# Kernel tuning notes

Hardware: AMD Instinct MI355X
Metric: run time of the kernel (lower is better)

The kernel has to match this reference:

```python
import jax, jax.numpy as jnp
import numpy as np

N_NODES = 100000


def _gcn_norm(edge_index, num_nodes):
    # add self loops, then symmetric normalization D^-1/2 (A+I) D^-1/2
    loops = jnp.arange(num_nodes, dtype=edge_index.dtype)
    src = jnp.concatenate([edge_index[0], loops])
    dst = jnp.concatenate([edge_index[1], loops])
    ones = jnp.ones(src.shape[0], dtype=jnp.float32)
    deg = jax.ops.segment_sum(ones, dst, num_segments=num_nodes)
    dinv = jnp.where(deg > 0, jax.lax.rsqrt(deg), 0.0)
    norm = dinv[src] * dinv[dst]  # [E+N]
    return src, dst, norm


def setup_inputs() -> dict:
    key = jax.random.key(0)
    k1, k2, k3, k4 = jax.random.split(key, 4)
    x = jax.random.normal(k1, (N_NODES, 512), dtype=jnp.float32)
    edge_index = jax.random.randint(k2, (2, 3200000), 0, N_NODES, dtype=jnp.int64)
    # SGConv linear: Linear(num_features=512, num_classes=40)
    W = jax.random.normal(k3, (40, 512), dtype=jnp.float32) / np.sqrt(512.0)
    b = jax.random.normal(k4, (40,), dtype=jnp.float32) * 0.01
    return {"x": x, "edge_index": edge_index, "W": W, "b": b}


def reference(x, edge_index, W, b):
    K = 2  # args.num_layers
    src, dst, norm = _gcn_norm(edge_index, N_NODES)
    h = x
    for _ in range(K):
        # SpMM: out[dst] += norm * h[src]
        h = jax.ops.segment_sum(norm[:, None] * h[src], dst, num_segments=N_NODES)
    logits = h @ W.T + b  # [N, num_classes]
    return jax.nn.log_softmax(logits, axis=1)
```

## Files before the change

kernel.cpp:

```cpp
#include <hip/hip_runtime.h>
#include <hip/hip_bf16.h>
#include <math.h>


#define NFEAT 512
#define NCLS  40
#define NBUCK_MAX 512
#define CAP   9728

typedef __attribute__((ext_vector_type(8))) short bf16x8;
typedef __attribute__((ext_vector_type(4))) float f32x4;

__device__ inline short f2bf(float f) {
    union { float f; unsigned u; } v; v.f = f;
    unsigned r = (v.u + 0x7FFFu + ((v.u >> 16) & 1u)) >> 16;
    return (short)r;
}
__device__ inline unsigned pack2bf(float a, float b) {
    return (unsigned)(unsigned short)f2bf(a) | ((unsigned)(unsigned short)f2bf(b) << 16);
}
__device__ inline float bflo(unsigned v) {
    union { unsigned u; float f; } r; r.u = v << 16; return r.f;
}
__device__ inline float bfhi(unsigned v) {
    union { unsigned u; float f; } r; r.u = v & 0xFFFF0000u; return r.f;
}


__global__ __launch_bounds__(256) void scat7_kernel(const int* __restrict__ src,
                                                    const int* __restrict__ dst,
                                                    int* __restrict__ bcursor,
                                                    unsigned* __restrict__ bco, int E) {
    __shared__ int h[NBUCK_MAX], h2[NBUCK_MAX], base[NBUCK_MAX];
    int t = threadIdx.x;
    h[t] = 0; h[t + 256] = 0; h2[t] = 0; h2[t + 256] = 0;
    __syncthreads();
    int cb = blockIdx.x * 2048;
    int d[8], s[8];
    bool m[8];
    #pragma unroll
    for (int u = 0; u < 8; ++u) {
        int e = cb + u * 256 + t;
        m[u] = e < E;
        d[u] = m[u] ? __builtin_nontemporal_load(dst + e) : 0;
        s[u] = m[u] ? __builtin_nontemporal_load(src + e) : 0;
        if (m[u]) atomicAdd(&h[d[u] >> 8], 1);
    }
    __syncthreads();
    #pragma unroll
    for (int b = 0; b < 2; ++b) {
        int bb = t + b * 256;
        if (h[bb]) base[bb] = bb * CAP + atomicAdd(&bcursor[bb], h[bb]);
    }
    __syncthreads();
    #pragma unroll
    for (int u = 0; u < 8; ++u) {
        if (m[u]) {
            int b = d[u] >> 8;
            int lp = atomicAdd(&h2[b], 1);
            bco[base[b] + lp] = ((unsigned)s[u] << 8) | (unsigned)(d[u] & 255);
        }
    }
}


__global__ __launch_bounds__(256) void sortb3_kernel(const unsigned* __restrict__ bco,
                                                     const int* __restrict__ bcursor,
                                                     int4* __restrict__ rowinfo,
                                                     float* __restrict__ dinv,
                                                     int* __restrict__ csr_src, int N) {
    __shared__ int deg[256], ex[256], sc[256];
    int b = blockIdx.x, t = threadIdx.x;
    int lo = b * 256;
    int nn = N - lo; if (nn > 256) nn = 256;
    int ebeg = b * CAP;
    int ecnt = bcursor[b];

    deg[t] = 0;
    __syncthreads();
    for (int i = t; i < ecnt; i += 256)
        atomicAdd(&deg[bco[ebeg + i] & 255u], 1);
    __syncthreads();
    int v = deg[t];
    sc[t] = v;
    __syncthreads();
    for (int off = 1; off < 256; off <<= 1) {
        int u = (t >= off) ? sc[t - off] : 0;
        __syncthreads();
        sc[t] += u;
        __syncthreads();
    }
    int ext = sc[t] - v;
    ex[t] = ext;
    if (t < nn) {
        float di = rsqrtf((float)(v + 1));
        int4 ri;
        ri.x = ebeg + ext;
        ri.y = v;
        ri.z = __float_as_int(di);
        ri.w = 0;
        rowinfo[lo + t] = ri;
        dinv[lo + t]    = di;
    }
    __syncthreads();
    for (int i = t; i < ecnt; i += 256) {
        unsigned e = bco[ebeg + i];
        int p = atomicAdd(&ex[e & 255u], 1);
        csr_src[ebeg + p] = (int)(e >> 8);
    }
}


__global__ void wfrag_kernel(const float* __restrict__ W, short* __restrict__ wfrag,
                             int* __restrict__ bcursor) {
    int i = blockIdx.x * blockDim.x + threadIdx.x;
    if (i < NBUCK_MAX) bcursor[i] = 0;
    if (i >= 16 * 3 * 64) return;
    int kc = i / 192, rem = i % 192, tile = rem / 64, lane = rem % 64;
    int c = tile * 16 + (lane & 15);
    int kbase = kc * 32 + ((lane >> 4) << 3);
    bf16x8 out;
    #pragma unroll
    for (int j = 0; j < 8; ++j) {
        float v = (c < NCLS) ? W[(size_t)c * NFEAT + kbase + j] : 0.f;
        out[j] = f2bf(v);
    }
    *(bf16x8*)(wfrag + (size_t)i * 8) = out;
}


__global__ __launch_bounds__(512) void gemm7_kernel(const float* __restrict__ x,
                                                    const short* __restrict__ wfrag,
                                                    const float* __restrict__ dinv,
                                                    unsigned short* __restrict__ zp, int n) {
    __shared__ short xl[2][128 * 40];
    int t = threadIdx.x;
    int w = t >> 6, l = t & 63;
    int lrow = l & 15, lk = l >> 4;
    int rowBase = blockIdx.x * 128;
    int srow = t >> 2, skq = t & 3;
    f32x4 acc0 = {0.f, 0.f, 0.f, 0.f}, acc1 = acc0, acc2 = acc0;
    const float* xrow = x + (size_t)(rowBase + srow) * NFEAT + skq * 8;
    bool srOK = (rowBase + srow) < n;
    int aoff = (w * 16 + lrow) * 40 + lk * 8;
    int doff = srow * 40 + skq * 8;

    {
        float4 v0 = make_float4(0.f, 0.f, 0.f, 0.f), v1 = v0;
        if (srOK) { const float4* xp = (const float4*)xrow; v0 = xp[0]; v1 = xp[1]; }
        bf16x8 bv;
        bv[0] = f2bf(v0.x); bv[1] = f2bf(v0.y); bv[2] = f2bf(v0.z); bv[3] = f2bf(v0.w);
        bv[4] = f2bf(v1.x); bv[5] = f2bf(v1.y); bv[6] = f2bf(v1.z); bv[7] = f2bf(v1.w);
        *(bf16x8*)&xl[0][doff] = bv;
    }
    __syncthreads();

    for (int kc = 0; kc < 16; ++kc) {
        int cur = kc & 1;
        float4 v0 = make_float4(0.f, 0.f, 0.f, 0.f), v1 = v0;
        if (kc < 15 && srOK) {
            const float4* xp = (const float4*)(xrow + (kc + 1) * 32);
            v0 = xp[0]; v1 = xp[1];
        }
        bf16x8 af = *(const bf16x8*)&xl[cur][aoff];
        const bf16x8* wf = (const bf16x8*)(wfrag + (size_t)kc * 3 * 64 * 8);
        bf16x8 b0 = wf[l];
        bf16x8 b1 = wf[64 + l];
        bf16x8 b2 = wf[128 + l];
        acc0 = __builtin_amdgcn_mfma_f32_16x16x32_bf16(af, b0, acc0, 0, 0, 0);
        acc1 = __builtin_amdgcn_mfma_f32_16x16x32_bf16(af, b1, acc1, 0, 0, 0);
        acc2 = __builtin_amdgcn_mfma_f32_16x16x32_bf16(af, b2, acc2, 0, 0, 0);
        if (kc < 15) {
            bf16x8 bv;
            bv[0] = f2bf(v0.x); bv[1] = f2bf(v0.y); bv[2] = f2bf(v0.z); bv[3] = f2bf(v0.w);
            bv[4] = f2bf(v1.x); bv[5] = f2bf(v1.y); bv[6] = f2bf(v1.z); bv[7] = f2bf(v1.w);
            *(bf16x8*)&xl[cur ^ 1][doff] = bv;
            __syncthreads();
        }
    }
    int r0 = rowBase + w * 16 + lk * 4;
    #pragma unroll
    for (int reg = 0; reg < 4; ++reg) {
        int row = r0 + reg;
        if (row < n) {
            float sc = dinv[row];
            unsigned short* zr = zp + (size_t)row * 64;
            zr[lrow]      = (unsigned short)f2bf(acc0[reg] * sc);
            zr[16 + lrow] = (unsigned short)f2bf(acc1[reg] * sc);
            zr[32 + lrow] = (lrow < 8) ? (unsigned short)f2bf(acc2[reg] * sc) : 0;
            zr[48 + lrow] = 0;
        }
    }
}


template <bool FINAL>
__global__ __launch_bounds__(256) void spmm12_kernel(const unsigned short* __restrict__ in,
                                                     const int4* __restrict__ rowinfo,
                                                     const int* __restrict__ csr,
                                                     const float* __restrict__ bias,
                                                     unsigned short* __restrict__ outP,
                                                     float* __restrict__ outF, int n) {
    int wv = (int)((blockIdx.x * (size_t)blockDim.x + threadIdx.x) >> 6);
    wv = __builtin_amdgcn_readfirstlane(wv);
    if (wv >= n) return;
    int lane = threadIdx.x & 63;
    int g  = lane >> 3;
    int oc = lane & 7;

    const char* rowb = (const char*)in + oc * 16;

    int4 ri = rowinfo[wv];
    int beg = ri.x, tot = ri.y;
    float dd = __int_as_float(ri.z);

    float a0 = 0.f, a1 = 0.f, a2 = 0.f, a3 = 0.f,
          a4 = 0.f, a5 = 0.f, a6 = 0.f, a7 = 0.f;

#define ACC_ADD(V)                                                     \
    { a0 += bflo((V).x); a1 += bfhi((V).x); a2 += bflo((V).y);         \
      a3 += bfhi((V).y); a4 += bflo((V).z); a5 += bfhi((V).z);         \
      a6 += bflo((V).w); a7 += bfhi((V).w); }

    if (g == 0) {
        uint4 v = *(const uint4*)(rowb + (size_t)wv * 128);
        ACC_ADD(v);
    }

    int j = 0;
    for (; j + 32 <= tot; j += 32) {
        int s0 = csr[beg + j + g];
        int s1 = csr[beg + j + 8 + g];
        int s2 = csr[beg + j + 16 + g];
        int s3 = csr[beg + j + 24 + g];
        uint4 v0 = *(const uint4*)(rowb + (size_t)s0 * 128);
        uint4 v1 = *(const uint4*)(rowb + (size_t)s1 * 128);
        uint4 v2 = *(const uint4*)(rowb + (size_t)s2 * 128);
        uint4 v3 = *(const uint4*)(rowb + (size_t)s3 * 128);
        ACC_ADD(v0); ACC_ADD(v1); ACC_ADD(v2); ACC_ADD(v3);
    }
    for (; j < tot; j += 8) {
        if (g < tot - j) {
            int s = csr[beg + j + g];
            uint4 v = *(const uint4*)(rowb + (size_t)s * 128);
            ACC_ADD(v);
        }
    }
#undef ACC_ADD

    #pragma unroll
    for (int off = 8; off <= 32; off <<= 1) {
        a0 += __shfl_xor(a0, off, 64); a1 += __shfl_xor(a1, off, 64);
        a2 += __shfl_xor(a2, off, 64); a3 += __shfl_xor(a3, off, 64);
        a4 += __shfl_xor(a4, off, 64); a5 += __shfl_xor(a5, off, 64);
        a6 += __shfl_xor(a6, off, 64); a7 += __shfl_xor(a7, off, 64);
    }

    if (!FINAL) {
        if (g == 0) {
            float s2 = dd * dd;
            uint4 o;
            o.x = pack2bf(a0 * s2, a1 * s2);
            o.y = pack2bf(a2 * s2, a3 * s2);
            o.z = pack2bf(a4 * s2, a5 * s2);
            o.w = pack2bf(a6 * s2, a7 * s2);
            *(uint4*)((char*)outP + (size_t)wv * 128 + oc * 16) = o;
        }
    } else {
        float b0 = 0.f, b1 = 0.f, b2 = 0.f, b3 = 0.f,
              b4 = 0.f, b5 = 0.f, b6 = 0.f, b7 = 0.f;
        if (oc < 5) {
            float4 q0 = ((const float4*)bias)[oc * 2];
            float4 q1 = ((const float4*)bias)[oc * 2 + 1];
            b0 = q0.x; b1 = q0.y; b2 = q0.z; b3 = q0.w;
            b4 = q1.x; b5 = q1.y; b6 = q1.z; b7 = q1.w;
        }
        bool valid = oc < 5;
        float v0 = valid ? a0 * dd + b0 : -INFINITY;
        float v1 = valid ? a1 * dd + b1 : -INFINITY;
        float v2 = valid ? a2 * dd + b2 : -INFINITY;
        float v3 = valid ? a3 * dd + b3 : -INFINITY;
        float v4 = valid ? a4 * dd + b4 : -INFINITY;
        float v5 = valid ? a5 * dd + b5 : -INFINITY;
        float v6 = valid ? a6 * dd + b6 : -INFINITY;
        float v7 = valid ? a7 * dd + b7 : -INFINITY;
        float m = fmaxf(fmaxf(fmaxf(v0, v1), fmaxf(v2, v3)),
                        fmaxf(fmaxf(v4, v5), fmaxf(v6, v7)));
        #pragma unroll
        for (int off = 1; off <= 4; off <<= 1) m = fmaxf(m, __shfl_xor(m, off, 64));
        float es = 0.f;
        if (valid)
            es = expf(v0 - m) + expf(v1 - m) + expf(v2 - m) + expf(v3 - m)
               + expf(v4 - m) + expf(v5 - m) + expf(v6 - m) + expf(v7 - m);
        #pragma unroll
        for (int off = 1; off <= 4; off <<= 1) es += __shfl_xor(es, off, 64);
        float lse = logf(es) + m;
        if (g == 0 && valid) {
            float* op = outF + (size_t)wv * NCLS + oc * 8;
            float4 o0 = make_float4(v0 - lse, v1 - lse, v2 - lse, v3 - lse);
            float4 o1 = make_float4(v4 - lse, v5 - lse, v6 - lse, v7 - lse);
            *(float4*)op = o0;
            *(float4*)(op + 4) = o1;
        }
    }
}


extern "C" void kernel_launch(void* const* d_in, const int* in_sizes, int n_in,
                              void* d_out, int out_size, void* d_ws, size_t ws_size,
                              hipStream_t stream) {
    const float* x  = (const float*)d_in[0];
    const int*   ei = (const int*)d_in[1];
    const float* W  = (const float*)d_in[2];
    const float* b  = (const float*)d_in[3];

    const int N = in_sizes[0] / NFEAT;
    const int E = in_sizes[1] / 2;
    const int* src = ei;
    const int* dst = ei + E;
    const int nbuck = (N + 255) >> 8;

    char* p = (char*)d_ws;
    auto alloc = [&](size_t bytes) -> void* {
        void* r = (void*)p;
        p += (bytes + 255) & ~(size_t)255;
        return r;
    };
    int*      bcursor = (int*)     alloc((size_t)NBUCK_MAX * 4);
    int4*     rowinfo = (int4*)    alloc((size_t)N * 16);
    float*    dinv    = (float*)   alloc((size_t)N * 4);
    unsigned* bco     = (unsigned*)alloc((size_t)nbuck * CAP * 4 + 64);
    int*      csr_src = (int*)     alloc((size_t)nbuck * CAP * 4 + 64);
    short*    wfrag   = (short*)   alloc((size_t)16 * 3 * 64 * 8 * 2);
    unsigned short* zp  = (unsigned short*)alloc((size_t)N * 64 * 2);
    unsigned short* h1p = (unsigned short*)alloc((size_t)N * 64 * 2);

    wfrag_kernel<<<12, 256, 0, stream>>>(W, wfrag, bcursor);

    int cb = (E + 2047) / 2048;
    scat7_kernel<<<cb, 256, 0, stream>>>(src, dst, bcursor, bco, E);
    sortb3_kernel<<<nbuck, 256, 0, stream>>>(bco, bcursor, rowinfo, dinv, csr_src, N);

    gemm7_kernel<<<(N + 127) / 128, 512, 0, stream>>>(x, wfrag, dinv, zp, N);

    int wb = (int)(((size_t)N * 64 + 255) / 256);
    spmm12_kernel<false><<<wb, 256, 0, stream>>>(zp, rowinfo, csr_src, b, h1p, nullptr, N);
    spmm12_kernel<true ><<<wb, 256, 0, stream>>>(h1p, rowinfo, csr_src, b, nullptr,
                                                 (float*)d_out, N);
}
```

Measured before the change: 259.1 us.

## Fuse edge scatter with x·W GEMM in one launch and defer dinv scaling

The edge bucketing scatter and the dense x·W^T GEMM now run as separate block ranges of a single kernel, so the memory-bound scatter and the GEMM can overlap instead of running back to back. GEMM blocks are shrunk to 64 rows with 256 threads so both roles share one launch shape. Since the GEMM no longer waits for degrees, the dinv row scaling moves into the sort kernel, which rescales zp in place after building the CSR. This adds an extra read-modify-write pass over zp in the sort kernel, and the smaller GEMM tiles may reuse the W fragments less.

```diff
diff --git a/kernel.cpp b/kernel.cpp
--- a/kernel.cpp
+++ b/kernel.cpp
@@ -24,90 +24,6 @@
 }
 __device__ inline float bfhi(unsigned v) {
     union { unsigned u; float f; } r; r.u = v & 0xFFFF0000u; return r.f;
-}
-
-
-__global__ __launch_bounds__(256) void scat7_kernel(const int* __restrict__ src,
-                                                    const int* __restrict__ dst,
-                                                    int* __restrict__ bcursor,
-                                                    unsigned* __restrict__ bco, int E) {
-    __shared__ int h[NBUCK_MAX], h2[NBUCK_MAX], base[NBUCK_MAX];
-    int t = threadIdx.x;
-    h[t] = 0; h[t + 256] = 0; h2[t] = 0; h2[t + 256] = 0;
-    __syncthreads();
-    int cb = blockIdx.x * 2048;
-    int d[8], s[8];
-    bool m[8];
-    #pragma unroll
-    for (int u = 0; u < 8; ++u) {
-        int e = cb + u * 256 + t;
-        m[u] = e < E;
-        d[u] = m[u] ? __builtin_nontemporal_load(dst + e) : 0;
-        s[u] = m[u] ? __builtin_nontemporal_load(src + e) : 0;
-        if (m[u]) atomicAdd(&h[d[u] >> 8], 1);
-    }
-    __syncthreads();
-    #pragma unroll
-    for (int b = 0; b < 2; ++b) {
-        int bb = t + b * 256;
-        if (h[bb]) base[bb] = bb * CAP + atomicAdd(&bcursor[bb], h[bb]);
-    }
-    __syncthreads();
-    #pragma unroll
-    for (int u = 0; u < 8; ++u) {
-        if (m[u]) {
-            int b = d[u] >> 8;
-            int lp = atomicAdd(&h2[b], 1);
-            bco[base[b] + lp] = ((unsigned)s[u] << 8) | (unsigned)(d[u] & 255);
-        }
-    }
-}
-
-
-__global__ __launch_bounds__(256) void sortb3_kernel(const unsigned* __restrict__ bco,
-                                                     const int* __restrict__ bcursor,
-                                                     int4* __restrict__ rowinfo,
-                                                     float* __restrict__ dinv,
-                                                     int* __restrict__ csr_src, int N) {
-    __shared__ int deg[256], ex[256], sc[256];
-    int b = blockIdx.x, t = threadIdx.x;
-    int lo = b * 256;
-    int nn = N - lo; if (nn > 256) nn = 256;
-    int ebeg = b * CAP;
-    int ecnt = bcursor[b];
-
-    deg[t] = 0;
-    __syncthreads();
-    for (int i = t; i < ecnt; i += 256)
-        atomicAdd(&deg[bco[ebeg + i] & 255u], 1);
-    __syncthreads();
-    int v = deg[t];
-    sc[t] = v;
-    __syncthreads();
-    for (int off = 1; off < 256; off <<= 1) {
-        int u = (t >= off) ? sc[t - off] : 0;
-        __syncthreads();
-        sc[t] += u;
-        __syncthreads();
-    }
-    int ext = sc[t] - v;
-    ex[t] = ext;
-    if (t < nn) {
-        float di = rsqrtf((float)(v + 1));
-        int4 ri;
-        ri.x = ebeg + ext;
-        ri.y = v;
-        ri.z = __float_as_int(di);
-        ri.w = 0;
-        rowinfo[lo + t] = ri;
-        dinv[lo + t]    = di;
-    }
-    __syncthreads();
-    for (int i = t; i < ecnt; i += 256) {
-        unsigned e = bco[ebeg + i];
-        int p = atomicAdd(&ex[e & 255u], 1);
-        csr_src[ebeg + p] = (int)(e >> 8);
-    }
 }
 
 
@@ -129,15 +45,57 @@
 }
 
 
-__global__ __launch_bounds__(512) void gemm7_kernel(const float* __restrict__ x,
-                                                    const short* __restrict__ wfrag,
-                                                    const float* __restrict__ dinv,
-                                                    unsigned short* __restrict__ zp, int n) {
-    __shared__ short xl[2][128 * 40];
+__global__ __launch_bounds__(256) void fused1_kernel(const int* __restrict__ src,
+                                                     const int* __restrict__ dst,
+                                                     int* __restrict__ bcursor,
+                                                     unsigned* __restrict__ bco, int E,
+                                                     int CB,
+                                                     const float* __restrict__ x,
+                                                     const short* __restrict__ wfrag,
+                                                     unsigned short* __restrict__ zp,
+                                                     int n) {
+    __shared__ __align__(16) char smem[2 * 64 * 40 * 2];
     int t = threadIdx.x;
+
+    if (blockIdx.x < (unsigned)CB) {
+        int* h    = (int*)smem;
+        int* h2   = h + NBUCK_MAX;
+        int* base = h2 + NBUCK_MAX;
+        h[t] = 0; h[t + 256] = 0; h2[t] = 0; h2[t + 256] = 0;
+        __syncthreads();
+        int cb = blockIdx.x * 2048;
+        int d[8], s[8];
+        bool m[8];
+        #pragma unroll
+        for (int u = 0; u < 8; ++u) {
+            int e = cb + u * 256 + t;
+            m[u] = e < E;
+            d[u] = m[u] ? __builtin_nontemporal_load(dst + e) : 0;
+            s[u] = m[u] ? __builtin_nontemporal_load(src + e) : 0;
+            if (m[u]) atomicAdd(&h[d[u] >> 8], 1);
+        }
+        __syncthreads();
+        #pragma unroll
+        for (int b = 0; b < 2; ++b) {
+            int bb = t + b * 256;
+            if (h[bb]) base[bb] = bb * CAP + atomicAdd(&bcursor[bb], h[bb]);
+        }
+        __syncthreads();
+        #pragma unroll
+        for (int u = 0; u < 8; ++u) {
+            if (m[u]) {
+                int b = d[u] >> 8;
+                int lp = atomicAdd(&h2[b], 1);
+                bco[base[b] + lp] = ((unsigned)s[u] << 8) | (unsigned)(d[u] & 255);
+            }
+        }
+        return;
+    }
+
+    short (*xl)[64 * 40] = (short (*)[64 * 40])smem;
     int w = t >> 6, l = t & 63;
     int lrow = l & 15, lk = l >> 4;
-    int rowBase = blockIdx.x * 128;
+    int rowBase = (blockIdx.x - CB) * 64;
     int srow = t >> 2, skq = t & 3;
     f32x4 acc0 = {0.f, 0.f, 0.f, 0.f}, acc1 = acc0, acc2 = acc0;
     const float* xrow = x + (size_t)(rowBase + srow) * NFEAT + skq * 8;
@@ -183,13 +141,66 @@
     for (int reg = 0; reg < 4; ++reg) {
         int row = r0 + reg;
         if (row < n) {
-            float sc = dinv[row];
             unsigned short* zr = zp + (size_t)row * 64;
-            zr[lrow]      = (unsigned short)f2bf(acc0[reg] * sc);
-            zr[16 + lrow] = (unsigned short)f2bf(acc1[reg] * sc);
-            zr[32 + lrow] = (lrow < 8) ? (unsigned short)f2bf(acc2[reg] * sc) : 0;
+            zr[lrow]      = (unsigned short)f2bf(acc0[reg]);
+            zr[16 + lrow] = (unsigned short)f2bf(acc1[reg]);
+            zr[32 + lrow] = (lrow < 8) ? (unsigned short)f2bf(acc2[reg]) : 0;
             zr[48 + lrow] = 0;
         }
+    }
+}
+
+
+__global__ __launch_bounds__(256) void sortb4_kernel(const unsigned* __restrict__ bco,
+                                                     const int* __restrict__ bcursor,
+                                                     int4* __restrict__ rowinfo,
+                                                     int* __restrict__ csr_src,
+                                                     unsigned short* __restrict__ zp,
+                                                     int N) {
+    __shared__ int deg[256], ex[256], sc[256];
+    int b = blockIdx.x, t = threadIdx.x;
+    int lo = b * 256;
+    int nn = N - lo; if (nn > 256) nn = 256;
+    int ebeg = b * CAP;
+    int ecnt = bcursor[b];
+
+    deg[t] = 0;
+    __syncthreads();
+    for (int i = t; i < ecnt; i += 256)
+        atomicAdd(&deg[bco[ebeg + i] & 255u], 1);
+    __syncthreads();
+    int v = deg[t];
+    sc[t] = v;
+    __syncthreads();
+    for (int off = 1; off < 256; off <<= 1) {
+        int u = (t >= off) ? sc[t - off] : 0;
+        __syncthreads();
+        sc[t] += u;
+        __syncthreads();
+    }
+    int ext = sc[t] - v;
+    ex[t] = ext;
+    if (t < nn) {
+        float di = rsqrtf((float)(v + 1));
+        int4 ri;
+        ri.x = ebeg + ext;
+        ri.y = v;
+        ri.z = __float_as_int(di);
+        ri.w = 0;
+        rowinfo[lo + t] = ri;
+    }
+    __syncthreads();
+    for (int i = t; i < ecnt; i += 256) {
+        unsigned e = bco[ebeg + i];
+        int p = atomicAdd(&ex[e & 255u], 1);
+        csr_src[ebeg + p] = (int)(e >> 8);
+    }
+    for (int idx = t; idx < nn * 32; idx += 256) {
+        int row = idx >> 5, c = idx & 31;
+        float di = rsqrtf((float)(deg[row] + 1));
+        unsigned* zr = (unsigned*)(zp + (size_t)(lo + row) * 64);
+        unsigned vv = zr[c];
+        zr[c] = pack2bf(bflo(vv) * di, bfhi(vv) * di);
     }
 }
 
@@ -328,7 +339,6 @@
     };
     int*      bcursor = (int*)     alloc((size_t)NBUCK_MAX * 4);
     int4*     rowinfo = (int4*)    alloc((size_t)N * 16);
-    float*    dinv    = (float*)   alloc((size_t)N * 4);
     unsigned* bco     = (unsigned*)alloc((size_t)nbuck * CAP * 4 + 64);
     int*      csr_src = (int*)     alloc((size_t)nbuck * CAP * 4 + 64);
     short*    wfrag   = (short*)   alloc((size_t)16 * 3 * 64 * 8 * 2);
@@ -337,11 +347,12 @@
 
     wfrag_kernel<<<12, 256, 0, stream>>>(W, wfrag, bcursor);
 
-    int cb = (E + 2047) / 2048;
-    scat7_kernel<<<cb, 256, 0, stream>>>(src, dst, bcursor, bco, E);
-    sortb3_kernel<<<nbuck, 256, 0, stream>>>(bco, bcursor, rowinfo, dinv, csr_src, N);
-
-    gemm7_kernel<<<(N + 127) / 128, 512, 0, stream>>>(x, wfrag, dinv, zp, N);
+    int CB = (E + 2047) / 2048;
+    int GB = (N + 63) / 64;
+    fused1_kernel<<<CB + GB, 256, 0, stream>>>(src, dst, bcursor, bco, E, CB,
+                                               x, wfrag, zp, N);
+
+    sortb4_kernel<<<nbuck, 256, 0, stream>>>(bco, bcursor, rowinfo, csr_src, zp, N);
 
     int wb = (int)(((size_t)N * 64 + 255) / 256);
     spmm12_kernel<false><<<wb, 256, 0, stream>>>(zp, rowinfo, csr_src, b, h1p, nullptr, N);
```

Result: slower. 265.2 us (+2.3%).
